# Optimization experiments

Measured on AMD Instinct MI355X. Metric: run time of the kernel, lower is better.

The kernel has to match this reference:

```python
import jax, jax.numpy as jnp
import numpy as np

OUT_F = 4096   # compressed rows; logical m = 2*OUT_F
IN_F = 2048    # compressed cols; logical k = 2*IN_F
BATCH = 4096   # n = input.shape[0]

# valid sorted 2-of-4 column patterns for 2:4 structured sparsity
_PAIR_LUT = jnp.array([[0, 1], [0, 2], [0, 3], [1, 2], [1, 3], [2, 3]], dtype=jnp.int32)


def setup_inputs() -> dict:
    key = jax.random.key(0)
    k1, k2, k3, k4 = jax.random.split(key, 4)
    weight = jax.random.normal(k1, (OUT_F, IN_F), dtype=jnp.float32)
    # vector (row) sparsity: keep 1 of every 2 logical row-vectors -> collision-free logical row ids
    row_bit = jax.random.randint(k2, (OUT_F,), 0, 2)
    indices = (2 * jnp.arange(OUT_F, dtype=jnp.int32) + row_bit.astype(jnp.int32))
    # 2:4 column sparsity: per group of 4 logical cols, keep 2 distinct sorted positions
    pat = jax.random.randint(k3, (OUT_F, IN_F // 2), 0, 6)
    metadata = _PAIR_LUT[pat].reshape(OUT_F, IN_F)  # [OUT_F, IN_F], values in 0..3
    inp = jax.random.normal(k4, (BATCH, 2 * IN_F), dtype=jnp.float32)
    return {"weight": weight, "indices": indices, "metadata": metadata, "input": inp}


def reference(weight, indices, metadata, input):
    # Decompress the dual structured-sparse weight to its logical dense form,
    # then compute W_logical @ input^T (spmm_dense_trans semantics).
    out_f, in_f = weight.shape
    m, k = 2 * out_f, 2 * in_f
    # logical column of each compressed element: group base 4*(c//2) + 2-bit metadata
    col = 4 * (jnp.arange(in_f, dtype=jnp.int32) // 2)[None, :] + metadata  # [out_f, in_f]
    W = jnp.zeros((m, k), dtype=weight.dtype).at[indices[:, None], col].set(weight)
    return W @ input.T  # [m, n] = [2*out_f, batch]
```

## Files before the change

### kernel.cpp

```cpp
#include <hip/hip_runtime.h>

#define OUT_F 4096
#define IN_F  2048
#define KLOG  4096
#define NB    4096
typedef unsigned long long ull;

typedef __bf16 bf16x8 __attribute__((ext_vector_type(8)));
typedef short  s16x8  __attribute__((ext_vector_type(8)));
typedef float  f32x4  __attribute__((ext_vector_type(4)));

__device__ __forceinline__ unsigned short f2bf(float f) {
    unsigned int u = __float_as_uint(f);
    u += 0x7fffu + ((u >> 16) & 1u);
    return (unsigned short)(u >> 16);
}

__device__ __forceinline__ void gload_lds16(const void* g, void* l) {
    __builtin_amdgcn_global_load_lds(
        (const __attribute__((address_space(1))) unsigned int*)g,
        (__attribute__((address_space(3))) unsigned int*)l, 16, 0, 0);
}

__global__ __launch_bounds__(256) void prep_kernel(
    const float* __restrict__ weight, const int* __restrict__ metadata,
    const float* __restrict__ input,
    unsigned short* __restrict__ wsA, unsigned short* __restrict__ wsB)
{
    const int b = blockIdx.x;
    if (b < 8192) {
        const int g = b * 256 + threadIdx.x;
        const int r = g >> 9;
        const int c = (g & 511) * 4;
        const float4 wv = *(const float4*)(weight   + (size_t)r * IN_F + c);
        const int4   mv = *(const int4*)  (metadata + (size_t)r * IN_F + c);
        ull v0 = ((ull)f2bf(wv.x) << (mv.x * 16)) | ((ull)f2bf(wv.y) << (mv.y * 16));
        ull v1 = ((ull)f2bf(wv.z) << (mv.z * 16)) | ((ull)f2bf(wv.w) << (mv.w * 16));
        ull* dst = (ull*)(wsA + (size_t)r * KLOG + 2 * c);
        dst[0] = v0; dst[1] = v1;
    } else {
        const int g = (b - 8192) * 256 + threadIdx.x;
        const size_t off = (size_t)g * 8;
        const float4 f0 = *(const float4*)(input + off);
        const float4 f1 = *(const float4*)(input + off + 4);
        ull v0 =  (ull)f2bf(f0.x) | ((ull)f2bf(f0.y) << 16) |
                 ((ull)f2bf(f0.z) << 32) | ((ull)f2bf(f0.w) << 48);
        ull v1 =  (ull)f2bf(f1.x) | ((ull)f2bf(f1.y) << 16) |
                 ((ull)f2bf(f1.z) << 32) | ((ull)f2bf(f1.w) << 48);
        ull* dst = (ull*)(wsB + off);
        dst[0] = v0; dst[1] = v1;
    }
}

__global__ __launch_bounds__(256) void gemm_kernel(
    const unsigned short* __restrict__ wsA, const unsigned short* __restrict__ wsB,
    const int* __restrict__ indices, float* __restrict__ out)
{
    __shared__ __align__(16) unsigned short As[128 * 32];
    __shared__ __align__(16) unsigned short Bs[128 * 32];

    const int tid  = threadIdx.x;
    const int lane = tid & 63;
    const int wave = tid >> 6;
    const int wm   = wave >> 1;
    const int wn   = wave & 1;
    const int l15  = lane & 15;
    const int quad = lane >> 4;

    const int r0 = blockIdx.y * 128;
    const int b0 = blockIdx.x * 128;

    const int srow  = wave * 32 + (lane >> 2);
    const int scolh = (lane & 3) * 8;
    const unsigned ldsA0 = wave * 2048;
    const unsigned short* gA = wsA + (size_t)(r0 + srow) * KLOG + scolh;
    const unsigned short* gB = wsB + (size_t)(b0 + srow) * KLOG + scolh;

    f32x4 acc[4][4];
#pragma unroll
    for (int i = 0; i < 4; ++i)
#pragma unroll
        for (int j = 0; j < 4; ++j)
            acc[i][j] = (f32x4){0.f, 0.f, 0.f, 0.f};

    for (int k0 = 0; k0 < KLOG; k0 += 32) {
        gload_lds16(gA + k0,             (char*)As + ldsA0);
        gload_lds16(gA + 16 * KLOG + k0, (char*)As + ldsA0 + 1024);
        gload_lds16(gB + k0,             (char*)Bs + ldsA0);
        gload_lds16(gB + 16 * KLOG + k0, (char*)Bs + ldsA0 + 1024);
        __syncthreads();

        bf16x8 a[4], b[4];
#pragma unroll
        for (int i = 0; i < 4; ++i)
            a[i] = __builtin_bit_cast(bf16x8,
                     *(const s16x8*)(As + (wm * 64 + i * 16 + l15) * 32 + quad * 8));
#pragma unroll
        for (int j = 0; j < 4; ++j)
            b[j] = __builtin_bit_cast(bf16x8,
                     *(const s16x8*)(Bs + (wn * 64 + j * 16 + l15) * 32 + quad * 8));
#pragma unroll
        for (int i = 0; i < 4; ++i)
#pragma unroll
            for (int j = 0; j < 4; ++j)
                acc[i][j] = __builtin_amdgcn_mfma_f32_16x16x32_bf16(
                                a[i], b[j], acc[i][j], 0, 0, 0);
        __syncthreads();
    }

#pragma unroll
    for (int i = 0; i < 4; ++i) {
#pragma unroll
        for (int t = 0; t < 4; ++t) {
            const int r = r0 + wm * 64 + i * 16 + quad * 4 + t;
            const int L = indices[r];
            const size_t base  = (size_t)L * NB;
            const size_t baseZ = (size_t)(L ^ 1) * NB;
#pragma unroll
            for (int j = 0; j < 4; ++j) {
                const int col = b0 + wn * 64 + j * 16 + l15;
                out[base  + col] = acc[i][j][t];
                out[baseZ + col] = 0.0f;
            }
        }
    }
}

__global__ __launch_bounds__(256) void spmm_dt_fallback(
    const float* __restrict__ weight, const int* __restrict__ indices,
    const int* __restrict__ metadata, const float* __restrict__ input,
    float* __restrict__ out)
{
    __shared__ __align__(16) unsigned short As[128][32];
    __shared__ __align__(16) unsigned short Bs[128][32];
    const int tid = threadIdx.x, lane = tid & 63, wave = tid >> 6;
    const int wm = wave >> 1, wn = wave & 1, l15 = lane & 15, quad = lane >> 4;
    const int r0 = blockIdx.y * 128, b0 = blockIdx.x * 128;
    f32x4 acc[4][4];
#pragma unroll
    for (int i = 0; i < 4; ++i)
#pragma unroll
        for (int j = 0; j < 4; ++j) acc[i][j] = (f32x4){0.f, 0.f, 0.f, 0.f};
    const int srow = tid >> 3, sgrp = tid & 7;
    for (int kk = 0; kk < KLOG / 32; ++kk) {
        const int c0 = kk * 16, k0 = kk * 32;
#pragma unroll
        for (int s = 0; s < 4; ++s) {
            const int row = srow + s * 32;
            const size_t off = (size_t)(r0 + row) * IN_F + c0 + 2 * sgrp;
            const float2 w = *(const float2*)(weight + off);
            const int2  md = *(const int2*)(metadata + off);
            *(ull*)(&As[row][4 * sgrp]) =
                ((ull)f2bf(w.x) << (md.x * 16)) | ((ull)f2bf(w.y) << (md.y * 16));
        }
#pragma unroll
        for (int s = 0; s < 4; ++s) {
            const int row = srow + s * 32;
            const float4 f = *(const float4*)(&input[(size_t)(b0 + row) * KLOG + k0 + sgrp * 4]);
            *(ull*)(&Bs[row][sgrp * 4]) =
                 (ull)f2bf(f.x) | ((ull)f2bf(f.y) << 16) |
                ((ull)f2bf(f.z) << 32) | ((ull)f2bf(f.w) << 48);
        }
        __syncthreads();
        bf16x8 a[4], b[4];
#pragma unroll
        for (int i = 0; i < 4; ++i)
            a[i] = __builtin_bit_cast(bf16x8, *(const s16x8*)(&As[wm * 64 + i * 16 + l15][quad * 8]));
#pragma unroll
        for (int j = 0; j < 4; ++j)
            b[j] = __builtin_bit_cast(bf16x8, *(const s16x8*)(&Bs[wn * 64 + j * 16 + l15][quad * 8]));
#pragma unroll
        for (int i = 0; i < 4; ++i)
#pragma unroll
            for (int j = 0; j < 4; ++j)
                acc[i][j] = __builtin_amdgcn_mfma_f32_16x16x32_bf16(a[i], b[j], acc[i][j], 0, 0, 0);
        __syncthreads();
    }
#pragma unroll
    for (int i = 0; i < 4; ++i)
#pragma unroll
        for (int t = 0; t < 4; ++t) {
            const int r = r0 + wm * 64 + i * 16 + quad * 4 + t;
            const int L = indices[r];
            const size_t base = (size_t)L * NB, baseZ = (size_t)(L ^ 1) * NB;
#pragma unroll
            for (int j = 0; j < 4; ++j) {
                const int col = b0 + wn * 64 + j * 16 + l15;
                out[base + col] = acc[i][j][t];
                out[baseZ + col] = 0.0f;
            }
        }
}

extern "C" void kernel_launch(void* const* d_in, const int* in_sizes, int n_in,
                              void* d_out, int out_size, void* d_ws, size_t ws_size,
                              hipStream_t stream) {
    const float* weight   = (const float*)d_in[0];
    const int*   indices  = (const int*)d_in[1];
    const int*   metadata = (const int*)d_in[2];
    const float* input    = (const float*)d_in[3];
    float*       out      = (float*)d_out;

    const size_t needA = (size_t)OUT_F * KLOG * 2;
    const size_t needB = (size_t)NB * KLOG * 2;
    if (ws_size >= needA + needB) {
        unsigned short* wsA = (unsigned short*)d_ws;
        unsigned short* wsB = wsA + (size_t)OUT_F * KLOG;
        prep_kernel<<<dim3(16384), dim3(256), 0, stream>>>(weight, metadata, input, wsA, wsB);
        gemm_kernel<<<dim3(NB / 128, OUT_F / 128), dim3(256), 0, stream>>>(wsA, wsB, indices, out);
    } else {
        spmm_dt_fallback<<<dim3(NB / 128, OUT_F / 128), dim3(256), 0, stream>>>(
            weight, indices, metadata, input, out);
    }
}
```

Measured before the change: 416.8 us.

## Switch GEMM to 32x32x16 MFMA with XOR-swizzled LDS and wider prep

```diff
diff --git a/kernel.cpp b/kernel.cpp
--- a/kernel.cpp
+++ b/kernel.cpp
@@ -5,10 +5,12 @@
 #define KLOG  4096
 #define NB    4096
 typedef unsigned long long ull;
+typedef ull ullx2 __attribute__((ext_vector_type(2)));
 
 typedef __bf16 bf16x8 __attribute__((ext_vector_type(8)));
 typedef short  s16x8  __attribute__((ext_vector_type(8)));
 typedef float  f32x4  __attribute__((ext_vector_type(4)));
+typedef float  f32x16 __attribute__((ext_vector_type(16)));
 
 __device__ __forceinline__ unsigned short f2bf(float f) {
     unsigned int u = __float_as_uint(f);
@@ -28,27 +30,38 @@
     unsigned short* __restrict__ wsA, unsigned short* __restrict__ wsB)
 {
     const int b = blockIdx.x;
-    if (b < 8192) {
+    if (b < 4096) {
         const int g = b * 256 + threadIdx.x;
-        const int r = g >> 9;
-        const int c = (g & 511) * 4;
-        const float4 wv = *(const float4*)(weight   + (size_t)r * IN_F + c);
-        const int4   mv = *(const int4*)  (metadata + (size_t)r * IN_F + c);
-        ull v0 = ((ull)f2bf(wv.x) << (mv.x * 16)) | ((ull)f2bf(wv.y) << (mv.y * 16));
-        ull v1 = ((ull)f2bf(wv.z) << (mv.z * 16)) | ((ull)f2bf(wv.w) << (mv.w * 16));
+        const int r = g >> 8;
+        const int c = (g & 255) * 8;
+        const size_t off = (size_t)r * IN_F + c;
+        const float4 w0 = *(const float4*)(weight + off);
+        const float4 w1 = *(const float4*)(weight + off + 4);
+        const int4   m0 = *(const int4*)(metadata + off);
+        const int4   m1 = *(const int4*)(metadata + off + 4);
+        ullx2 v01, v23;
+        v01.x = ((ull)f2bf(w0.x) << (m0.x * 16)) | ((ull)f2bf(w0.y) << (m0.y * 16));
+        v01.y = ((ull)f2bf(w0.z) << (m0.z * 16)) | ((ull)f2bf(w0.w) << (m0.w * 16));
+        v23.x = ((ull)f2bf(w1.x) << (m1.x * 16)) | ((ull)f2bf(w1.y) << (m1.y * 16));
+        v23.y = ((ull)f2bf(w1.z) << (m1.z * 16)) | ((ull)f2bf(w1.w) << (m1.w * 16));
         ull* dst = (ull*)(wsA + (size_t)r * KLOG + 2 * c);
-        dst[0] = v0; dst[1] = v1;
+        *(ullx2*)(dst)     = v01;
+        *(ullx2*)(dst + 2) = v23;
     } else {
-        const int g = (b - 8192) * 256 + threadIdx.x;
-        const size_t off = (size_t)g * 8;
+        const int g = (b - 4096) * 256 + threadIdx.x;
+        const size_t off = (size_t)g * 16;
         const float4 f0 = *(const float4*)(input + off);
         const float4 f1 = *(const float4*)(input + off + 4);
-        ull v0 =  (ull)f2bf(f0.x) | ((ull)f2bf(f0.y) << 16) |
-                 ((ull)f2bf(f0.z) << 32) | ((ull)f2bf(f0.w) << 48);
-        ull v1 =  (ull)f2bf(f1.x) | ((ull)f2bf(f1.y) << 16) |
-                 ((ull)f2bf(f1.z) << 32) | ((ull)f2bf(f1.w) << 48);
+        const float4 f2 = *(const float4*)(input + off + 8);
+        const float4 f3 = *(const float4*)(input + off + 12);
+        ullx2 v01, v23;
+        v01.x =  (ull)f2bf(f0.x) | ((ull)f2bf(f0.y) << 16) | ((ull)f2bf(f0.z) << 32) | ((ull)f2bf(f0.w) << 48);
+        v01.y =  (ull)f2bf(f1.x) | ((ull)f2bf(f1.y) << 16) | ((ull)f2bf(f1.z) << 32) | ((ull)f2bf(f1.w) << 48);
+        v23.x =  (ull)f2bf(f2.x) | ((ull)f2bf(f2.y) << 16) | ((ull)f2bf(f2.z) << 32) | ((ull)f2bf(f2.w) << 48);
+        v23.y =  (ull)f2bf(f3.x) | ((ull)f2bf(f3.y) << 16) | ((ull)f2bf(f3.z) << 32) | ((ull)f2bf(f3.w) << 48);
         ull* dst = (ull*)(wsB + off);
-        dst[0] = v0; dst[1] = v1;
+        *(ullx2*)(dst)     = v01;
+        *(ullx2*)(dst + 2) = v23;
     }
 }
 
@@ -64,62 +77,74 @@
     const int wave = tid >> 6;
     const int wm   = wave >> 1;
     const int wn   = wave & 1;
-    const int l15  = lane & 15;
-    const int quad = lane >> 4;
+    const int l31  = lane & 31;
+    const int h    = lane >> 5;
 
     const int r0 = blockIdx.y * 128;
     const int b0 = blockIdx.x * 128;
 
-    const int srow  = wave * 32 + (lane >> 2);
-    const int scolh = (lane & 3) * 8;
-    const unsigned ldsA0 = wave * 2048;
-    const unsigned short* gA = wsA + (size_t)(r0 + srow) * KLOG + scolh;
-    const unsigned short* gB = wsB + (size_t)(b0 + srow) * KLOG + scolh;
-
-    f32x4 acc[4][4];
-#pragma unroll
-    for (int i = 0; i < 4; ++i)
-#pragma unroll
-        for (int j = 0; j < 4; ++j)
-            acc[i][j] = (f32x4){0.f, 0.f, 0.f, 0.f};
+    const int srow   = wave * 32 + (lane >> 2);
+    const int scol16 = (lane & 3) ^ ((lane >> 2) & 3);
+    const unsigned ldsOff = wave * 2048;
+    const unsigned short* gA = wsA + (size_t)(r0 + srow) * KLOG + scol16 * 8;
+    const unsigned short* gB = wsB + (size_t)(b0 + srow) * KLOG + scol16 * 8;
+
+    f32x16 acc[2][2];
+#pragma unroll
+    for (int i = 0; i < 2; ++i)
+#pragma unroll
+        for (int j = 0; j < 2; ++j)
+#pragma unroll
+            for (int e = 0; e < 16; ++e) acc[i][j][e] = 0.f;
 
     for (int k0 = 0; k0 < KLOG; k0 += 32) {
-        gload_lds16(gA + k0,             (char*)As + ldsA0);
-        gload_lds16(gA + 16 * KLOG + k0, (char*)As + ldsA0 + 1024);
-        gload_lds16(gB + k0,             (char*)Bs + ldsA0);
-        gload_lds16(gB + 16 * KLOG + k0, (char*)Bs + ldsA0 + 1024);
-        __syncthreads();
-
-        bf16x8 a[4], b[4];
-#pragma unroll
-        for (int i = 0; i < 4; ++i)
-            a[i] = __builtin_bit_cast(bf16x8,
-                     *(const s16x8*)(As + (wm * 64 + i * 16 + l15) * 32 + quad * 8));
-#pragma unroll
-        for (int j = 0; j < 4; ++j)
-            b[j] = __builtin_bit_cast(bf16x8,
-                     *(const s16x8*)(Bs + (wn * 64 + j * 16 + l15) * 32 + quad * 8));
-#pragma unroll
-        for (int i = 0; i < 4; ++i)
-#pragma unroll
-            for (int j = 0; j < 4; ++j)
-                acc[i][j] = __builtin_amdgcn_mfma_f32_16x16x32_bf16(
-                                a[i], b[j], acc[i][j], 0, 0, 0);
-        __syncthreads();
-    }
-
-#pragma unroll
-    for (int i = 0; i < 4; ++i) {
-#pragma unroll
-        for (int t = 0; t < 4; ++t) {
-            const int r = r0 + wm * 64 + i * 16 + quad * 4 + t;
-            const int L = indices[r];
+        gload_lds16(gA + k0,             (char*)As + ldsOff);
+        gload_lds16(gA + 16 * KLOG + k0, (char*)As + ldsOff + 1024);
+        gload_lds16(gB + k0,             (char*)Bs + ldsOff);
+        gload_lds16(gB + 16 * KLOG + k0, (char*)Bs + ldsOff + 1024);
+        __syncthreads();
+
+        bf16x8 a[2][2], b[2][2];
+#pragma unroll
+        for (int mi = 0; mi < 2; ++mi)
+#pragma unroll
+            for (int kh = 0; kh < 2; ++kh) {
+                const int row = wm * 64 + mi * 32 + l31;
+                const int phys = (kh * 2 + h) ^ (row & 3);
+                a[mi][kh] = __builtin_bit_cast(bf16x8, *(const s16x8*)(As + row * 32 + phys * 8));
+            }
+#pragma unroll
+        for (int nj = 0; nj < 2; ++nj)
+#pragma unroll
+            for (int kh = 0; kh < 2; ++kh) {
+                const int row = wn * 64 + nj * 32 + l31;
+                const int phys = (kh * 2 + h) ^ (row & 3);
+                b[nj][kh] = __builtin_bit_cast(bf16x8, *(const s16x8*)(Bs + row * 32 + phys * 8));
+            }
+
+#pragma unroll
+        for (int kh = 0; kh < 2; ++kh)
+#pragma unroll
+            for (int mi = 0; mi < 2; ++mi)
+#pragma unroll
+                for (int nj = 0; nj < 2; ++nj)
+                    acc[mi][nj] = __builtin_amdgcn_mfma_f32_32x32x16_bf16(
+                                      a[mi][kh], b[nj][kh], acc[mi][nj], 0, 0, 0);
+        __syncthreads();
+    }
+
+#pragma unroll
+    for (int mi = 0; mi < 2; ++mi) {
+#pragma unroll
+        for (int reg = 0; reg < 16; ++reg) {
+            const int rloc = wm * 64 + mi * 32 + (reg & 3) + 8 * (reg >> 2) + 4 * h;
+            const int L = indices[r0 + rloc];
             const size_t base  = (size_t)L * NB;
             const size_t baseZ = (size_t)(L ^ 1) * NB;
 #pragma unroll
-            for (int j = 0; j < 4; ++j) {
-                const int col = b0 + wn * 64 + j * 16 + l15;
-                out[base  + col] = acc[i][j][t];
+            for (int nj = 0; nj < 2; ++nj) {
+                const int col = b0 + wn * 64 + nj * 32 + l31;
+                out[base  + col] = acc[mi][nj][reg];
                 out[baseZ + col] = 0.0f;
             }
         }
@@ -206,7 +231,7 @@
     if (ws_size >= needA + needB) {
         unsigned short* wsA = (unsigned short*)d_ws;
         unsigned short* wsB = wsA + (size_t)OUT_F * KLOG;
-        prep_kernel<<<dim3(16384), dim3(256), 0, stream>>>(weight, metadata, input, wsA, wsB);
+        prep_kernel<<<dim3(8192), dim3(256), 0, stream>>>(weight, metadata, input, wsA, wsB);
         gemm_kernel<<<dim3(NB / 128, OUT_F / 128), dim3(256), 0, stream>>>(wsA, wsB, indices, out);
     } else {
         spmm_dt_fallback<<<dim3(NB / 128, OUT_F / 128), dim3(256), 0, stream>>>(
```

New measurement: 391.0 us. 6.2% less time.
